# Kernel optimization log

Hardware: AMD Instinct MI355X
Metric: run time of the kernel (lower is better)

Reference implementation:

```python
import jax, jax.numpy as jnp
import numpy as np

NBOXES = 4096
MAX_BS = 128
NDIM = 3
NPAIRS = 8192
INV4PI = 0.07957747154594767  # 1/(4*pi), 3D Laplace kernel constant


def setup_inputs() -> dict:
    key = jax.random.key(0)
    k1, k2, k3, k4 = jax.random.split(key, 4)
    q_vec = jax.random.normal(k1, (NBOXES, MAX_BS), dtype=jnp.float32)
    XX_list = jax.random.uniform(k2, (NBOXES, MAX_BS, NDIM), dtype=jnp.float32)
    bs_list = jax.random.randint(k3, (NBOXES,), 0, MAX_BS, dtype=jnp.int32)
    uq_boxes = jax.random.randint(k4, (NPAIRS, 2), 0, NBOXES, dtype=jnp.int32)
    return {"q_vec": q_vec, "XX_list": XX_list, "bs_list": bs_list, "uq_boxes": uq_boxes}


def reference(q_vec, XX_list, bs_list, uq_boxes):
    # Batched gather-kernel-matvec-scatter translation (addto_translation with
    # self_bool=False, kappa=0 => 3D Laplace kernel 1/(4*pi*r)).
    nboxes, max_bs = q_vec.shape
    u_boxes = uq_boxes[:, 0]
    q_boxes = uq_boxes[:, 1]

    Xu = XX_list[u_boxes]  # [P, B, 3] gather target points
    Xq = XX_list[q_boxes]  # [P, B, 3] gather source points

    # pairwise squared distances without materializing [P,B,B,3] diffs
    nu = jnp.sum(Xu * Xu, axis=-1)  # [P, B]
    nq = jnp.sum(Xq * Xq, axis=-1)  # [P, B]
    r2 = nu[:, :, None] + nq[:, None, :] - 2.0 * jnp.einsum('pid,pjd->pij', Xu, Xq)
    r2 = jnp.maximum(r2, 0.0)
    nz = r2 > 0.0
    K = jnp.where(nz, INV4PI / jnp.sqrt(jnp.where(nz, r2, 1.0)), 0.0)  # [P, B, B]

    cols = jnp.arange(max_bs, dtype=jnp.int32)
    col_mask = (cols[None, :] < bs_list[q_boxes][:, None]).astype(q_vec.dtype)  # valid src pts
    row_mask = (cols[None, :] < bs_list[u_boxes][:, None]).astype(q_vec.dtype)  # valid trg pts

    qv = q_vec[q_boxes] * col_mask                         # gather + zero_col_bnd
    out = jnp.einsum('pij,pj->pi', K, qv) * row_mask       # batched kernel matvec

    u_vec = jnp.zeros_like(q_vec).at[u_boxes].add(out)     # index_add_ scatter
    return u_vec
```

## Files before the change

kernel.cpp:

```cpp
#include <hip/hip_runtime.h>

#define MAX_BS 128
#define INV4PI 0.07957747154594767f

__global__ __launch_bounds__(128) void fmm_scalar_kernel(
    const float* __restrict__ q_vec,
    const float* __restrict__ XX,
    const int*   __restrict__ bs_list,
    const int2*  __restrict__ uq_boxes,
    float*       __restrict__ out)
{
    const int p = blockIdx.x;
    const int t = threadIdx.x;

    const int2 uq = uq_boxes[p];
    const int u = __builtin_amdgcn_readfirstlane(uq.x);
    const int q = __builtin_amdgcn_readfirstlane(uq.y);
    const int bs_u = bs_list[u];
    const int bs_q = bs_list[q];

    if (t >= bs_u || bs_q == 0) return;

    const float* __restrict__ Xu = XX + (size_t)u * (MAX_BS * 3);
    const float xu = Xu[3 * t + 0];
    const float yu = Xu[3 * t + 1];
    const float zu = Xu[3 * t + 2];

    const float* __restrict__ Xq = XX + (size_t)q * (MAX_BS * 3);
    const float* __restrict__ qv = q_vec + (size_t)q * MAX_BS;

    float acc = 0.0f;
    if (u != q) {
#pragma unroll 8
        for (int j = 0; j < bs_q; ++j) {
            const float sx = Xq[3 * j + 0];
            const float sy = Xq[3 * j + 1];
            const float sz = Xq[3 * j + 2];
            const float w  = qv[j];
            const float dx = xu - sx;
            const float dy = yu - sy;
            const float dz = zu - sz;
            const float r2 = dx * dx + dy * dy + dz * dz;
            acc = fmaf(w, __builtin_amdgcn_rsqf(r2), acc);
        }
    } else {
#pragma unroll 4
        for (int j = 0; j < bs_q; ++j) {
            const float sx = Xq[3 * j + 0];
            const float sy = Xq[3 * j + 1];
            const float sz = Xq[3 * j + 2];
            const float w  = qv[j];
            const float dx = xu - sx;
            const float dy = yu - sy;
            const float dz = zu - sz;
            const float r2 = dx * dx + dy * dy + dz * dz;
            float rinv = __builtin_amdgcn_rsqf(r2);
            rinv = (r2 > 0.0f) ? rinv : 0.0f;
            acc = fmaf(w, rinv, acc);
        }
    }

    atomicAdd(out + (size_t)u * MAX_BS + t, acc * INV4PI);
}

extern "C" void kernel_launch(void* const* d_in, const int* in_sizes, int n_in,
                              void* d_out, int out_size, void* d_ws, size_t ws_size,
                              hipStream_t stream) {
    const float* q_vec    = (const float*)d_in[0];
    const float* XX_list  = (const float*)d_in[1];
    const int*   bs_list  = (const int*)d_in[2];
    const int2*  uq_boxes = (const int2*)d_in[3];
    float* out = (float*)d_out;

    const int npairs = in_sizes[3] / 2;

    hipMemsetAsync(d_out, 0, (size_t)out_size * sizeof(float), stream);

    fmm_scalar_kernel<<<npairs, 128, 0, stream>>>(
        q_vec, XX_list, bs_list, uq_boxes, out);
}
```

Measured before the change: 85.97 us.

## Split source range across waves and compute two targets per thread

Each block's two waves now each process half of the source points, and every thread accumulates two target rows, so each loaded source coordinate feeds two distance evaluations. The main loop is explicitly batched by 8 loads before compute to expose memory-level parallelism. This is meant to cut per-thread source-load overhead and the serial loop length. In exchange, each output element now receives two atomic adds, and lanes whose rows fall beyond bs_u do wasted compute.

Measured after the change: 92.00 us. 1.07x slower.

```diff
diff --git a/kernel.cpp b/kernel.cpp
--- a/kernel.cpp
+++ b/kernel.cpp
@@ -3,7 +3,7 @@
 #define MAX_BS 128
 #define INV4PI 0.07957747154594767f
 
-__global__ __launch_bounds__(128) void fmm_scalar_kernel(
+__global__ __launch_bounds__(128) void fmm_split_kernel(
     const float* __restrict__ q_vec,
     const float* __restrict__ XX,
     const int*   __restrict__ bs_list,
@@ -11,56 +11,82 @@
     float*       __restrict__ out)
 {
     const int p = blockIdx.x;
-    const int t = threadIdx.x;
+    const int h = threadIdx.x >> 6;
+    const int t = threadIdx.x & 63;
 
     const int2 uq = uq_boxes[p];
     const int u = __builtin_amdgcn_readfirstlane(uq.x);
     const int q = __builtin_amdgcn_readfirstlane(uq.y);
     const int bs_u = bs_list[u];
     const int bs_q = bs_list[q];
+    if (bs_u == 0) return;
 
-    if (t >= bs_u || bs_q == 0) return;
+    const int hs = (bs_q + 1) >> 1;
+    const int j0 = h * hs;
+    const int j1 = (bs_q < j0 + hs) ? bs_q : (j0 + hs);
+    if (j0 >= j1) return;
 
-    const float* __restrict__ Xu = XX + (size_t)u * (MAX_BS * 3);
-    const float xu = Xu[3 * t + 0];
-    const float yu = Xu[3 * t + 1];
-    const float zu = Xu[3 * t + 2];
+    const int r0 = 2 * t;
+    const float* __restrict__ Xu = XX + (size_t)u * (MAX_BS * 3) + 6 * t;
+    const float x0 = Xu[0], y0 = Xu[1], z0 = Xu[2];
+    const float x1 = Xu[3], y1 = Xu[4], z1 = Xu[5];
 
     const float* __restrict__ Xq = XX + (size_t)q * (MAX_BS * 3);
     const float* __restrict__ qv = q_vec + (size_t)q * MAX_BS;
 
-    float acc = 0.0f;
+    float acc0 = 0.0f, acc1 = 0.0f;
+
     if (u != q) {
-#pragma unroll 8
-        for (int j = 0; j < bs_q; ++j) {
-            const float sx = Xq[3 * j + 0];
-            const float sy = Xq[3 * j + 1];
-            const float sz = Xq[3 * j + 2];
+        int j = j0;
+        for (; j + 8 <= j1; j += 8) {
+            float sx[8], sy[8], sz[8], w[8];
+#pragma unroll
+            for (int c = 0; c < 8; ++c) {
+                sx[c] = Xq[3 * (j + c) + 0];
+                sy[c] = Xq[3 * (j + c) + 1];
+                sz[c] = Xq[3 * (j + c) + 2];
+                w[c]  = qv[j + c];
+            }
+#pragma unroll
+            for (int c = 0; c < 8; ++c) {
+                const float dx0 = x0 - sx[c], dy0 = y0 - sy[c], dz0 = z0 - sz[c];
+                const float r20 = fmaf(dx0, dx0, fmaf(dy0, dy0, dz0 * dz0));
+                acc0 = fmaf(w[c], __builtin_amdgcn_rsqf(r20), acc0);
+                const float dx1 = x1 - sx[c], dy1 = y1 - sy[c], dz1 = z1 - sz[c];
+                const float r21 = fmaf(dx1, dx1, fmaf(dy1, dy1, dz1 * dz1));
+                acc1 = fmaf(w[c], __builtin_amdgcn_rsqf(r21), acc1);
+            }
+        }
+        for (; j < j1; ++j) {
+            const float sx = Xq[3 * j + 0], sy = Xq[3 * j + 1], sz = Xq[3 * j + 2];
             const float w  = qv[j];
-            const float dx = xu - sx;
-            const float dy = yu - sy;
-            const float dz = zu - sz;
-            const float r2 = dx * dx + dy * dy + dz * dz;
-            acc = fmaf(w, __builtin_amdgcn_rsqf(r2), acc);
+            const float dx0 = x0 - sx, dy0 = y0 - sy, dz0 = z0 - sz;
+            const float r20 = fmaf(dx0, dx0, fmaf(dy0, dy0, dz0 * dz0));
+            acc0 = fmaf(w, __builtin_amdgcn_rsqf(r20), acc0);
+            const float dx1 = x1 - sx, dy1 = y1 - sy, dz1 = z1 - sz;
+            const float r21 = fmaf(dx1, dx1, fmaf(dy1, dy1, dz1 * dz1));
+            acc1 = fmaf(w, __builtin_amdgcn_rsqf(r21), acc1);
         }
     } else {
-#pragma unroll 4
-        for (int j = 0; j < bs_q; ++j) {
-            const float sx = Xq[3 * j + 0];
-            const float sy = Xq[3 * j + 1];
-            const float sz = Xq[3 * j + 2];
+        for (int j = j0; j < j1; ++j) {
+            const float sx = Xq[3 * j + 0], sy = Xq[3 * j + 1], sz = Xq[3 * j + 2];
             const float w  = qv[j];
-            const float dx = xu - sx;
-            const float dy = yu - sy;
-            const float dz = zu - sz;
-            const float r2 = dx * dx + dy * dy + dz * dz;
-            float rinv = __builtin_amdgcn_rsqf(r2);
-            rinv = (r2 > 0.0f) ? rinv : 0.0f;
-            acc = fmaf(w, rinv, acc);
+            const float dx0 = x0 - sx, dy0 = y0 - sy, dz0 = z0 - sz;
+            const float r20 = fmaf(dx0, dx0, fmaf(dy0, dy0, dz0 * dz0));
+            float rv0 = __builtin_amdgcn_rsqf(r20);
+            rv0 = (r20 > 0.0f) ? rv0 : 0.0f;
+            acc0 = fmaf(w, rv0, acc0);
+            const float dx1 = x1 - sx, dy1 = y1 - sy, dz1 = z1 - sz;
+            const float r21 = fmaf(dx1, dx1, fmaf(dy1, dy1, dz1 * dz1));
+            float rv1 = __builtin_amdgcn_rsqf(r21);
+            rv1 = (r21 > 0.0f) ? rv1 : 0.0f;
+            acc1 = fmaf(w, rv1, acc1);
         }
     }
 
-    atomicAdd(out + (size_t)u * MAX_BS + t, acc * INV4PI);
+    float* orow = out + (size_t)u * MAX_BS + r0;
+    if (r0     < bs_u) atomicAdd(orow + 0, acc0 * INV4PI);
+    if (r0 + 1 < bs_u) atomicAdd(orow + 1, acc1 * INV4PI);
 }
 
 extern "C" void kernel_launch(void* const* d_in, const int* in_sizes, int n_in,
@@ -76,6 +102,6 @@
 
     hipMemsetAsync(d_out, 0, (size_t)out_size * sizeof(float), stream);
 
-    fmm_scalar_kernel<<<npairs, 128, 0, stream>>>(
+    fmm_split_kernel<<<npairs, 128, 0, stream>>>(
         q_vec, XX_list, bs_list, uq_boxes, out);
 }
```
